# Kernel optimization log

Hardware: AMD Instinct MI355X
Metric: run time of the kernel (lower is better)

Reference implementation:

```python
import jax, jax.numpy as jnp
import numpy as np

N, E, IN, H, OUT = 50000, 800000, 256, 128, 64


def setup_inputs() -> dict:
    key = jax.random.key(0)
    ks = jax.random.split(key, 4)
    x = jax.random.normal(ks[0], (N, IN), dtype=jnp.float32)
    edge_index = jax.random.randint(ks[1], (2, E), 0, N, dtype=jnp.int64)
    W1 = jax.random.normal(ks[2], (IN, H), dtype=jnp.float32) / np.float32(np.sqrt(IN))
    b1 = jnp.zeros((H,), jnp.float32)
    W2 = jax.random.normal(ks[3], (H, OUT), dtype=jnp.float32) / np.float32(np.sqrt(H))
    b2 = jnp.zeros((OUT,), jnp.float32)
    return {"x": x, "edge_index": edge_index, "W1": W1, "b1": b1, "W2": W2, "b2": b2}


def _gcn_conv(x, W, b, src, dst, norm, n):
    # PyG GCNConv: linear transform, then symmetric-normalized aggregation, then bias
    h = x @ W                                        # [n, d_out]
    agg = jax.ops.segment_sum(h[src] * norm[:, None], dst, num_segments=n)
    return agg + b


def reference(x, edge_index, W1, b1, W2, b2):
    n = x.shape[0]
    loop = jnp.arange(n, dtype=edge_index.dtype)
    # add self-loops (GCNConv default add_self_loops=True)
    src = jnp.concatenate([edge_index[0], loop])
    dst = jnp.concatenate([edge_index[1], loop])
    # symmetric normalization deg^{-1/2} A_hat deg^{-1/2}
    deg = jax.ops.segment_sum(jnp.ones(src.shape, jnp.float32), dst, num_segments=n)
    dinv = jnp.where(deg > 0, jax.lax.rsqrt(deg), 0.0)
    norm = dinv[src] * dinv[dst]                     # [E + n]
    h = jax.nn.relu(_gcn_conv(x, W1, b1, src, dst, norm, n))
    return _gcn_conv(h, W2, b2, src, dst, norm, n)
```

## Files before the change

### kernel.cpp

```cpp
#include <hip/hip_runtime.h>


#define DI 256
#define DH 128
#define DO 64
#define NBC 98
#define EPB 8192
#define P4CAP 12288

typedef unsigned short ushort;
typedef unsigned int uint;
using bf16x8 = __attribute__((ext_vector_type(8))) short;
using f32x4  = __attribute__((ext_vector_type(4))) float;

__device__ __forceinline__ ushort f2b(float f) {
    union { float f; uint u; } v; v.f = f;
    uint r = (v.u + 0x7fffu + ((v.u >> 16) & 1u)) >> 16;
    return (ushort)r;
}
__device__ __forceinline__ float blo(uint v) { return __uint_as_float(v << 16); }
__device__ __forceinline__ float bhi(uint v) { return __uint_as_float(v & 0xffff0000u); }

__global__ __launch_bounds__(256) void hist_k(const int* __restrict__ dst,
                                              int* __restrict__ hist, int E) {
    __shared__ int lh[NBC];
    const int blk = blockIdx.x;
    for (int i = threadIdx.x; i < NBC; i += 256) lh[i] = 0;
    __syncthreads();
    const int base = blk * EPB, end = min(base + EPB, E);
    for (int e = base + threadIdx.x; e < end; e += 256)
        atomicAdd(&lh[dst[e] >> 9], 1);
    __syncthreads();
    for (int i = threadIdx.x; i < NBC; i += 256) hist[blk * NBC + i] = lh[i];
}

__global__ void scan_mat(int* __restrict__ hist, int* __restrict__ boff,
                         int* __restrict__ off, int nbp, int n, int E) {
    __shared__ int mat[NBC * NBC];
    __shared__ int tot[NBC], bo[NBC];
    const int tid = threadIdx.x;
    const int tote = nbp * NBC;
    for (int i = tid; i < tote; i += 256) mat[i] = hist[i];
    __syncthreads();
    if (tid < NBC) {
        int run = 0;
        for (int b = 0; b < nbp; ++b) {
            int v = mat[b * NBC + tid];
            mat[b * NBC + tid] = run;
            run += v;
        }
        tot[tid] = run;
    }
    __syncthreads();
    if (tid == 0) {
        int r = 0;
        for (int c = 0; c < NBC; ++c) { bo[c] = r; r += tot[c]; }
        boff[NBC] = r;
        off[n] = E;
    }
    __syncthreads();
    if (tid < NBC) boff[tid] = bo[tid];
    for (int i = tid; i < tote; i += 256) hist[i] = mat[i] + bo[i % NBC];
}

__global__ __launch_bounds__(256) void part_k(const int* __restrict__ src,
                                              const int* __restrict__ dst,
                                              const int* __restrict__ hist,
                                              uint* __restrict__ pairs, int E) {
    __shared__ int cur[NBC];
    const int blk = blockIdx.x;
    for (int i = threadIdx.x; i < NBC; i += 256) cur[i] = hist[blk * NBC + i];
    __syncthreads();
    const int base = blk * EPB, end = min(base + EPB, E);
    for (int e = base + threadIdx.x; e < end; e += 256) {
        int d = dst[e], s = src[e];
        int slot = atomicAdd(&cur[d >> 9], 1);
        pairs[slot] = ((uint)s << 9) | (uint)(d & 511);
    }
}

__global__ __launch_bounds__(256) void bucket_k(const uint* __restrict__ pairs,
                                                const int* __restrict__ boff,
                                                int* __restrict__ off,
                                                float* __restrict__ dinv,
                                                int* __restrict__ csr, int n) {
    __shared__ int lh[512], lcur[512], tsum[256];
    __shared__ int sorted[P4CAP];
    const int tid = threadIdx.x;
    const int cb = blockIdx.x;
    const int b0 = boff[cb], b1 = boff[cb + 1];
    const int cnt = b1 - b0;
    lh[tid] = 0; lh[tid + 256] = 0;
    __syncthreads();
    for (int i = tid; i < cnt; i += 256) atomicAdd(&lh[pairs[b0 + i] & 511], 1);
    __syncthreads();
    const int s0 = lh[2 * tid], s1 = lh[2 * tid + 1];
    const int s = s0 + s1;
    tsum[tid] = s;
    __syncthreads();
    for (int o = 1; o < 256; o <<= 1) {
        int t = (tid >= o) ? tsum[tid - o] : 0;
        __syncthreads();
        tsum[tid] += t;
        __syncthreads();
    }
    const int ex = tsum[tid] - s;
    lcur[2 * tid] = ex; lcur[2 * tid + 1] = ex + s0;
    {
        int node = cb * 512 + 2 * tid;
        if (node < n)     { off[node]     = b0 + ex;      dinv[node]     = rsqrtf((float)s0 + 1.f); }
        if (node + 1 < n) { off[node + 1] = b0 + ex + s0; dinv[node + 1] = rsqrtf((float)s1 + 1.f); }
    }
    __syncthreads();
    for (int i = tid; i < cnt; i += 256) {
        uint v = pairs[b0 + i];
        int slot = atomicAdd(&lcur[v & 511], 1);
        if (slot < P4CAP) sorted[slot] = (int)(v >> 9);
    }
    __syncthreads();
    const int cs = min(cnt, P4CAP);
    for (int i = tid; i < cs; i += 256) csr[b0 + i] = sorted[i];
}

__global__ void wt_cvt(const float* __restrict__ W, ushort* __restrict__ Wt, int K, int M) {
    int idx = blockIdx.x * 256 + threadIdx.x;
    if (idx < K * M) {
        int m = idx / K, k = idx % K;
        Wt[idx] = f2b(W[(long)k * M + m]);
    }
}

template<int K, int M, bool INF32>
__global__ __launch_bounds__(256) void mfma_gemm(const void* __restrict__ Xv,
                                                 const ushort* __restrict__ Wt,
                                                 const float* __restrict__ dinv,
                                                 ushort* __restrict__ Y, int n) {
    constexpr int ROWB = K * 2;
    constexpr int CT = M / 64;
    __shared__ ushort Xs[64 * K];
    const int t = threadIdx.x;
    const int r0 = blockIdx.x * 64;

    {
        const int row = t & 63, c = t >> 6;
        const int gr = r0 + row;
        if (INF32) {
            const float4* Xr = (const float4*)((const float*)Xv + (long)gr * K);
#pragma unroll
            for (int j = 0; j < K / 32; ++j) {
                float4 a, b;
                if (gr < n) {
                    a = Xr[c * (K / 16) + 2 * j];
                    b = Xr[c * (K / 16) + 2 * j + 1];
                } else {
                    a = make_float4(0.f, 0.f, 0.f, 0.f); b = a;
                }
                ushort u[8] = {f2b(a.x), f2b(a.y), f2b(a.z), f2b(a.w),
                               f2b(b.x), f2b(b.y), f2b(b.z), f2b(b.w)};
                int byte = row * ROWB + c * (K / 2) + j * 16;
                byte ^= (row & 7) << 4;
                *(uint4*)((char*)Xs + byte) = *(const uint4*)u;
            }
        } else {
            const uint4* Xr = (const uint4*)((const ushort*)Xv + (long)gr * K);
#pragma unroll
            for (int j = 0; j < K / 32; ++j) {
                uint4 v = make_uint4(0u, 0u, 0u, 0u);
                if (gr < n) v = Xr[c * (K / 32) + j];
                int byte = row * ROWB + c * (K / 2) + j * 16;
                byte ^= (row & 7) << 4;
                *(uint4*)((char*)Xs + byte) = v;
            }
        }
    }
    __syncthreads();

    const int w  = t >> 6;
    const int l  = t & 63;
    const int lr = l & 15;
    const int lg = l >> 4;
    f32x4 acc[4][CT] = {};

#pragma unroll
    for (int ks = 0; ks < K / 32; ++ks) {
        bf16x8 bfr[CT];
#pragma unroll
        for (int ct = 0; ct < CT; ++ct) {
            int col = w * (M / 4) + ct * 16 + lr;
            bfr[ct] = *(const bf16x8*)&Wt[(long)col * K + ks * 32 + lg * 8];
        }
        bf16x8 afr[4];
#pragma unroll
        for (int rt = 0; rt < 4; ++rt) {
            int row = rt * 16 + lr;
            int byte = row * ROWB + ks * 64 + lg * 16;
            byte ^= (row & 7) << 4;
            afr[rt] = *(const bf16x8*)((const char*)Xs + byte);
        }
#pragma unroll
        for (int rt = 0; rt < 4; ++rt)
#pragma unroll
            for (int ct = 0; ct < CT; ++ct)
                acc[rt][ct] = __builtin_amdgcn_mfma_f32_16x16x32_bf16(
                    afr[rt], bfr[ct], acc[rt][ct], 0, 0, 0);
    }

#pragma unroll
    for (int rt = 0; rt < 4; ++rt)
#pragma unroll
        for (int i = 0; i < 4; ++i) {
            int gr2 = r0 + rt * 16 + lg * 4 + i;
            if (gr2 < n) {
                float dv = dinv[gr2];
#pragma unroll
                for (int ct = 0; ct < CT; ++ct) {
                    int col = w * (M / 4) + ct * 16 + lr;
                    Y[(long)gr2 * M + col] = f2b(dv * acc[rt][ct][i]);
                }
            }
        }
}

template<int M, bool RELU, bool OUTF32>
__global__ void gather_fin(const int* __restrict__ off, const int* __restrict__ csr,
                           const ushort* __restrict__ Hs, const float* __restrict__ dinv,
                           const float* __restrict__ b, void* __restrict__ Yv, int n) {
    constexpr int G = M / 8;
    constexpr int NPB = 256 / G;
    int g = threadIdx.x / G;
    int j = threadIdx.x % G;
    int i = blockIdx.x * NPB + g;
    if (i >= n) return;
    const uint4* H4 = (const uint4*)Hs;
    float acc[8];
    {
        uint4 s = H4[(long)i * G + j];
        acc[0] = blo(s.x); acc[1] = bhi(s.x);
        acc[2] = blo(s.y); acc[3] = bhi(s.y);
        acc[4] = blo(s.z); acc[5] = bhi(s.z);
        acc[6] = blo(s.w); acc[7] = bhi(s.w);
    }
    int k = off[i], ke = off[i + 1];
    for (; k + 3 < ke; k += 4) {
        int s0 = csr[k], s1 = csr[k + 1], s2 = csr[k + 2], s3 = csr[k + 3];
        uint4 a0 = H4[(long)s0 * G + j];
        uint4 a1 = H4[(long)s1 * G + j];
        uint4 a2 = H4[(long)s2 * G + j];
        uint4 a3 = H4[(long)s3 * G + j];
        acc[0] += blo(a0.x) + blo(a1.x) + blo(a2.x) + blo(a3.x);
        acc[1] += bhi(a0.x) + bhi(a1.x) + bhi(a2.x) + bhi(a3.x);
        acc[2] += blo(a0.y) + blo(a1.y) + blo(a2.y) + blo(a3.y);
        acc[3] += bhi(a0.y) + bhi(a1.y) + bhi(a2.y) + bhi(a3.y);
        acc[4] += blo(a0.z) + blo(a1.z) + blo(a2.z) + blo(a3.z);
        acc[5] += bhi(a0.z) + bhi(a1.z) + bhi(a2.z) + bhi(a3.z);
        acc[6] += blo(a0.w) + blo(a1.w) + blo(a2.w) + blo(a3.w);
        acc[7] += bhi(a0.w) + bhi(a1.w) + bhi(a2.w) + bhi(a3.w);
    }
    for (; k < ke; ++k) {
        uint4 a = H4[(long)csr[k] * G + j];
        acc[0] += blo(a.x); acc[1] += bhi(a.x);
        acc[2] += blo(a.y); acc[3] += bhi(a.y);
        acc[4] += blo(a.z); acc[5] += bhi(a.z);
        acc[6] += blo(a.w); acc[7] += bhi(a.w);
    }
    float di = dinv[i];
    float4 b0 = ((const float4*)b)[j * 2];
    float4 b1 = ((const float4*)b)[j * 2 + 1];
    float r[8];
    r[0] = di * acc[0] + b0.x; r[1] = di * acc[1] + b0.y;
    r[2] = di * acc[2] + b0.z; r[3] = di * acc[3] + b0.w;
    r[4] = di * acc[4] + b1.x; r[5] = di * acc[5] + b1.y;
    r[6] = di * acc[6] + b1.z; r[7] = di * acc[7] + b1.w;
    if (RELU) {
#pragma unroll
        for (int m = 0; m < 8; ++m) r[m] = fmaxf(r[m], 0.f);
    }
    if (OUTF32) {
        float* Y = (float*)Yv;
        *(float4*)&Y[(long)i * M + j * 8]     = make_float4(r[0], r[1], r[2], r[3]);
        *(float4*)&Y[(long)i * M + j * 8 + 4] = make_float4(r[4], r[5], r[6], r[7]);
    } else {
        ushort* Y = (ushort*)Yv;
        uint4 o;
        o.x = (uint)f2b(r[0]) | ((uint)f2b(r[1]) << 16);
        o.y = (uint)f2b(r[2]) | ((uint)f2b(r[3]) << 16);
        o.z = (uint)f2b(r[4]) | ((uint)f2b(r[5]) << 16);
        o.w = (uint)f2b(r[6]) | ((uint)f2b(r[7]) << 16);
        *(uint4*)&Y[(long)i * M + j * 8] = o;
    }
}

extern "C" void kernel_launch(void* const* d_in, const int* in_sizes, int n_in,
                              void* d_out, int out_size, void* d_ws, size_t ws_size,
                              hipStream_t stream) {
    const float* x  = (const float*)d_in[0];
    const int*   ei = (const int*)d_in[1];
    const float* W1 = (const float*)d_in[2];
    const float* b1 = (const float*)d_in[3];
    const float* W2 = (const float*)d_in[4];
    const float* b2 = (const float*)d_in[5];
    float* out = (float*)d_out;

    const int n = in_sizes[0] / DI;
    const int E = in_sizes[1] / 2;
    const int* src = ei;
    const int* dst = ei + E;
    const int np  = ((n + 255) / 256) * 256;
    const int nbp = (E + EPB - 1) / EPB;
    const int nbc = (n + 511) >> 9;

    int*    hist  = (int*)d_ws;
    int*    boff  = hist + NBC * NBC;
    int*    off   = boff + 128;
    float*  dinv  = (float*)(off + np + 256);
    int*    csr   = (int*)(dinv + np);
    uint*   pairs = (uint*)(csr + E);
    ushort* w1t   = (ushort*)(pairs + E);
    ushort* w2t   = w1t + DH * DI;
    ushort* h0s   = w2t + DO * DH;
    ushort* h     = h0s + (size_t)n * DH;
    ushort* h1s   = h0s;

    hist_k<<<nbp, 256, 0, stream>>>(dst, hist, E);
    scan_mat<<<1, 256, 0, stream>>>(hist, boff, off, nbp, n, E);
    part_k<<<nbp, 256, 0, stream>>>(src, dst, hist, pairs, E);
    bucket_k<<<nbc, 256, 0, stream>>>(pairs, boff, off, dinv, csr, n);

    wt_cvt<<<(DI * DH + 255) / 256, 256, 0, stream>>>(W1, w1t, DI, DH);
    wt_cvt<<<(DH * DO + 255) / 256, 256, 0, stream>>>(W2, w2t, DH, DO);

    const int gblk = (n + 63) / 64;
    mfma_gemm<DI, DH, true><<<gblk, 256, 0, stream>>>(x, w1t, dinv, h0s, n);
    gather_fin<DH, true, false><<<(n + 15) / 16, 256, 0, stream>>>(off, csr, h0s, dinv, b1, h, n);
    mfma_gemm<DH, DO, false><<<gblk, 256, 0, stream>>>(h, w2t, dinv, h1s, n);
    gather_fin<DO, false, true><<<(n + 31) / 32, 256, 0, stream>>>(off, csr, h1s, dinv, b2, out, n);
}
```

Measured before the change: 234.1 us.

## Use one wavefront per node in gather and coalesce GEMM input loads

The aggregation kernel now assigns a full 64-lane wavefront to each destination node. Several lane groups each process a strided share of the neighbor list, and their partial sums are combined with xor shuffles. This exposes more independent loads per node and hides gather latency, at the cost of more blocks and idle lanes on low-degree nodes. The GEMM staging load is remapped so that 4 consecutive threads read one row contiguously, which improves coalescing. The two weight-conversion launches are merged into one kernel.

```diff
diff --git a/kernel.cpp b/kernel.cpp
--- a/kernel.cpp
+++ b/kernel.cpp
@@ -122,11 +122,16 @@
     for (int i = tid; i < cs; i += 256) csr[b0 + i] = sorted[i];
 }
 
-__global__ void wt_cvt(const float* __restrict__ W, ushort* __restrict__ Wt, int K, int M) {
+__global__ void wt_cvt2(const float* __restrict__ W1, ushort* __restrict__ W1t,
+                        const float* __restrict__ W2, ushort* __restrict__ W2t) {
     int idx = blockIdx.x * 256 + threadIdx.x;
-    if (idx < K * M) {
-        int m = idx / K, k = idx % K;
-        Wt[idx] = f2b(W[(long)k * M + m]);
+    if (idx < DI * DH) {
+        int m = idx / DI, k = idx % DI;
+        W1t[idx] = f2b(W1[(long)k * DH + m]);
+    }
+    if (idx < DH * DO) {
+        int m = idx / DH, k = idx % DH;
+        W2t[idx] = f2b(W2[(long)k * DO + m]);
     }
 }
 
@@ -142,32 +147,30 @@
     const int r0 = blockIdx.x * 64;
 
     {
-        const int row = t & 63, c = t >> 6;
+        const int row = t >> 2, q = t & 3;
         const int gr = r0 + row;
         if (INF32) {
-            const float4* Xr = (const float4*)((const float*)Xv + (long)gr * K);
+            const float* Xr = (const float*)Xv + (long)gr * K;
 #pragma unroll
             for (int j = 0; j < K / 32; ++j) {
-                float4 a, b;
+                float4 a = make_float4(0.f, 0.f, 0.f, 0.f), b = a;
                 if (gr < n) {
-                    a = Xr[c * (K / 16) + 2 * j];
-                    b = Xr[c * (K / 16) + 2 * j + 1];
-                } else {
-                    a = make_float4(0.f, 0.f, 0.f, 0.f); b = a;
+                    a = *(const float4*)&Xr[q * 8 + j * 32];
+                    b = *(const float4*)&Xr[q * 8 + j * 32 + 4];
                 }
                 ushort u[8] = {f2b(a.x), f2b(a.y), f2b(a.z), f2b(a.w),
                                f2b(b.x), f2b(b.y), f2b(b.z), f2b(b.w)};
-                int byte = row * ROWB + c * (K / 2) + j * 16;
+                int byte = row * ROWB + q * 16 + j * 64;
                 byte ^= (row & 7) << 4;
                 *(uint4*)((char*)Xs + byte) = *(const uint4*)u;
             }
         } else {
-            const uint4* Xr = (const uint4*)((const ushort*)Xv + (long)gr * K);
+            const ushort* Xr = (const ushort*)Xv + (long)gr * K;
 #pragma unroll
             for (int j = 0; j < K / 32; ++j) {
                 uint4 v = make_uint4(0u, 0u, 0u, 0u);
-                if (gr < n) v = Xr[c * (K / 32) + j];
-                int byte = row * ROWB + c * (K / 2) + j * 16;
+                if (gr < n) v = *(const uint4*)&Xr[q * 8 + j * 32];
+                int byte = row * ROWB + q * 16 + j * 64;
                 byte ^= (row & 7) << 4;
                 *(uint4*)((char*)Xs + byte) = v;
             }
@@ -222,71 +225,67 @@
 }
 
 template<int M, bool RELU, bool OUTF32>
-__global__ void gather_fin(const int* __restrict__ off, const int* __restrict__ csr,
-                           const ushort* __restrict__ Hs, const float* __restrict__ dinv,
-                           const float* __restrict__ b, void* __restrict__ Yv, int n) {
-    constexpr int G = M / 8;
-    constexpr int NPB = 256 / G;
-    int g = threadIdx.x / G;
-    int j = threadIdx.x % G;
-    int i = blockIdx.x * NPB + g;
+__global__ __launch_bounds__(256) void gather_wave(const int* __restrict__ off,
+                                                   const int* __restrict__ csr,
+                                                   const ushort* __restrict__ Hs,
+                                                   const float* __restrict__ dinv,
+                                                   const float* __restrict__ b,
+                                                   void* __restrict__ Yv, int n) {
+    constexpr int LPG = M / 8;
+    constexpr int GR  = 64 / LPG;
+    const int wv = threadIdx.x >> 6;
+    const int ln = threadIdx.x & 63;
+    const int grp = ln / LPG;
+    const int j   = ln % LPG;
+    const int i = blockIdx.x * 4 + wv;
     if (i >= n) return;
     const uint4* H4 = (const uint4*)Hs;
-    float acc[8];
-    {
-        uint4 s = H4[(long)i * G + j];
-        acc[0] = blo(s.x); acc[1] = bhi(s.x);
-        acc[2] = blo(s.y); acc[3] = bhi(s.y);
-        acc[4] = blo(s.z); acc[5] = bhi(s.z);
-        acc[6] = blo(s.w); acc[7] = bhi(s.w);
-    }
-    int k = off[i], ke = off[i + 1];
-    for (; k + 3 < ke; k += 4) {
-        int s0 = csr[k], s1 = csr[k + 1], s2 = csr[k + 2], s3 = csr[k + 3];
-        uint4 a0 = H4[(long)s0 * G + j];
-        uint4 a1 = H4[(long)s1 * G + j];
-        uint4 a2 = H4[(long)s2 * G + j];
-        uint4 a3 = H4[(long)s3 * G + j];
-        acc[0] += blo(a0.x) + blo(a1.x) + blo(a2.x) + blo(a3.x);
-        acc[1] += bhi(a0.x) + bhi(a1.x) + bhi(a2.x) + bhi(a3.x);
-        acc[2] += blo(a0.y) + blo(a1.y) + blo(a2.y) + blo(a3.y);
-        acc[3] += bhi(a0.y) + bhi(a1.y) + bhi(a2.y) + bhi(a3.y);
-        acc[4] += blo(a0.z) + blo(a1.z) + blo(a2.z) + blo(a3.z);
-        acc[5] += bhi(a0.z) + bhi(a1.z) + bhi(a2.z) + bhi(a3.z);
-        acc[6] += blo(a0.w) + blo(a1.w) + blo(a2.w) + blo(a3.w);
-        acc[7] += bhi(a0.w) + bhi(a1.w) + bhi(a2.w) + bhi(a3.w);
-    }
-    for (; k < ke; ++k) {
-        uint4 a = H4[(long)csr[k] * G + j];
+    float acc[8] = {0.f, 0.f, 0.f, 0.f, 0.f, 0.f, 0.f, 0.f};
+    const int k0 = off[i], ke = off[i + 1];
+    for (int k = k0 + grp; k < ke; k += GR) {
+        uint4 a = H4[(long)csr[k] * LPG + j];
         acc[0] += blo(a.x); acc[1] += bhi(a.x);
         acc[2] += blo(a.y); acc[3] += bhi(a.y);
         acc[4] += blo(a.z); acc[5] += bhi(a.z);
         acc[6] += blo(a.w); acc[7] += bhi(a.w);
     }
-    float di = dinv[i];
-    float4 b0 = ((const float4*)b)[j * 2];
-    float4 b1 = ((const float4*)b)[j * 2 + 1];
-    float r[8];
-    r[0] = di * acc[0] + b0.x; r[1] = di * acc[1] + b0.y;
-    r[2] = di * acc[2] + b0.z; r[3] = di * acc[3] + b0.w;
-    r[4] = di * acc[4] + b1.x; r[5] = di * acc[5] + b1.y;
-    r[6] = di * acc[6] + b1.z; r[7] = di * acc[7] + b1.w;
-    if (RELU) {
-#pragma unroll
-        for (int m = 0; m < 8; ++m) r[m] = fmaxf(r[m], 0.f);
-    }
-    if (OUTF32) {
-        float* Y = (float*)Yv;
-        *(float4*)&Y[(long)i * M + j * 8]     = make_float4(r[0], r[1], r[2], r[3]);
-        *(float4*)&Y[(long)i * M + j * 8 + 4] = make_float4(r[4], r[5], r[6], r[7]);
-    } else {
-        ushort* Y = (ushort*)Yv;
-        uint4 o;
-        o.x = (uint)f2b(r[0]) | ((uint)f2b(r[1]) << 16);
-        o.y = (uint)f2b(r[2]) | ((uint)f2b(r[3]) << 16);
-        o.z = (uint)f2b(r[4]) | ((uint)f2b(r[5]) << 16);
-        o.w = (uint)f2b(r[6]) | ((uint)f2b(r[7]) << 16);
-        *(uint4*)&Y[(long)i * M + j * 8] = o;
+    if (grp == 0) {
+        uint4 a = H4[(long)i * LPG + j];
+        acc[0] += blo(a.x); acc[1] += bhi(a.x);
+        acc[2] += blo(a.y); acc[3] += bhi(a.y);
+        acc[4] += blo(a.z); acc[5] += bhi(a.z);
+        acc[6] += blo(a.w); acc[7] += bhi(a.w);
+    }
+#pragma unroll
+    for (int o = LPG; o < 64; o <<= 1)
+#pragma unroll
+        for (int m = 0; m < 8; ++m) acc[m] += __shfl_xor(acc[m], o, 64);
+    if (grp == 0) {
+        float di = dinv[i];
+        float4 b0 = ((const float4*)b)[j * 2];
+        float4 b1 = ((const float4*)b)[j * 2 + 1];
+        float r[8];
+        r[0] = di * acc[0] + b0.x; r[1] = di * acc[1] + b0.y;
+        r[2] = di * acc[2] + b0.z; r[3] = di * acc[3] + b0.w;
+        r[4] = di * acc[4] + b1.x; r[5] = di * acc[5] + b1.y;
+        r[6] = di * acc[6] + b1.z; r[7] = di * acc[7] + b1.w;
+        if (RELU) {
+#pragma unroll
+            for (int m = 0; m < 8; ++m) r[m] = fmaxf(r[m], 0.f);
+        }
+        if (OUTF32) {
+            float* Y = (float*)Yv;
+            *(float4*)&Y[(long)i * M + j * 8]     = make_float4(r[0], r[1], r[2], r[3]);
+            *(float4*)&Y[(long)i * M + j * 8 + 4] = make_float4(r[4], r[5], r[6], r[7]);
+        } else {
+            ushort* Y = (ushort*)Yv;
+            uint4 o;
+            o.x = (uint)f2b(r[0]) | ((uint)f2b(r[1]) << 16);
+            o.y = (uint)f2b(r[2]) | ((uint)f2b(r[3]) << 16);
+            o.z = (uint)f2b(r[4]) | ((uint)f2b(r[5]) << 16);
+            o.w = (uint)f2b(r[6]) | ((uint)f2b(r[7]) << 16);
+            *(uint4*)&Y[(long)i * M + j * 8] = o;
+        }
     }
 }
 
@@ -325,13 +324,11 @@
     scan_mat<<<1, 256, 0, stream>>>(hist, boff, off, nbp, n, E);
     part_k<<<nbp, 256, 0, stream>>>(src, dst, hist, pairs, E);
     bucket_k<<<nbc, 256, 0, stream>>>(pairs, boff, off, dinv, csr, n);
-
-    wt_cvt<<<(DI * DH + 255) / 256, 256, 0, stream>>>(W1, w1t, DI, DH);
-    wt_cvt<<<(DH * DO + 255) / 256, 256, 0, stream>>>(W2, w2t, DH, DO);
+    wt_cvt2<<<(DI * DH + 255) / 256, 256, 0, stream>>>(W1, w1t, W2, w2t);
 
     const int gblk = (n + 63) / 64;
     mfma_gemm<DI, DH, true><<<gblk, 256, 0, stream>>>(x, w1t, dinv, h0s, n);
-    gather_fin<DH, true, false><<<(n + 15) / 16, 256, 0, stream>>>(off, csr, h0s, dinv, b1, h, n);
+    gather_wave<DH, true, false><<<(n + 3) / 4, 256, 0, stream>>>(off, csr, h0s, dinv, b1, h, n);
     mfma_gemm<DH, DO, false><<<gblk, 256, 0, stream>>>(h, w2t, dinv, h1s, n);
-    gather_fin<DO, false, true><<<(n + 31) / 32, 256, 0, stream>>>(off, csr, h1s, dinv, b2, out, n);
-}
+    gather_wave<DO, false, true><<<(n + 3) / 4, 256, 0, stream>>>(off, csr, h1s, dinv, b2, out, n);
+}
```

Result: no change. 237.9 us (+1.6%).
